# Performance work log

Hardware: AMD Instinct MI355X
Metric: run time of the kernel (lower is better)

Reference implementation:

```python
import jax, jax.numpy as jnp
import numpy as np

L, H, D, DK, FF = 3, 8, 128, 16, 512  # layers, heads, embed, key/val dim, ffn hidden
B, N, F_IN, OUT = 32, 512, 16, 3
SCALE = 1.0 / np.sqrt(DK)


def setup_inputs() -> dict:
    key = jax.random.key(0)
    ks = jax.random.split(key, 16)
    x = jax.random.normal(ks[0], (B, N, F_IN), dtype=jnp.float32)
    m = jax.random.randint(ks[1], (B, N, N), 0, 2).astype(jnp.int32)
    # guarantee each query attends to at least itself (avoid all -inf rows)
    m = jnp.maximum(m, jnp.eye(N, dtype=jnp.int32)[None])
    def u(k, shape, fan):
        s = 1.0 / np.sqrt(fan)
        return jax.random.uniform(k, shape, jnp.float32, -s, s)
    return {
        "x": x, "mask": m,
        "We": u(ks[2], (F_IN, D), D),
        "Wq": u(ks[3], (L, H, D, DK), DK),
        "Wk": u(ks[4], (L, H, D, DK), DK),
        "Wv": u(ks[5], (L, H, D, DK), DK),
        "Wout": u(ks[6], (L, H, DK, D), D),
        "Wff1": u(ks[7], (L, D, FF), D),
        "bff1": u(ks[8], (L, FF), D),
        "Wff2": u(ks[9], (L, FF, D), FF),
        "bff2": u(ks[10], (L, D), FF),
        "Wp": u(ks[11], (D, D), D),
        "Wr": u(ks[12], (2 * D, OUT), 2 * D),
        "br": u(ks[13], (OUT,), 2 * D),
    }


def reference(x, mask, We, Wq, Wk, Wv, Wout, Wff1, bff1, Wff2, bff2, Wp, Wr, br):
    mb = mask.astype(bool)[None]  # [1,B,N,N] broadcast over heads
    h = jax.nn.relu(x @ We)  # initial embedding [B,N,D]
    for l in range(L):
        # multi-head attention with additive skip
        Q = jnp.einsum('bnd,hdk->hbnk', h, Wq[l])
        K = jnp.einsum('bnd,hdk->hbnk', h, Wk[l])
        V = jnp.einsum('bnd,hdk->hbnk', h, Wv[l])
        compat = SCALE * jnp.einsum('hbqk,hbnk->hbqn', Q, K)  # [H,B,N,N]
        compat = jnp.where(mb, compat, -jnp.inf)
        attn = jax.nn.softmax(compat, axis=-1)
        # note: torch's attn.clone()[...] = 0 is a no-op, so no re-zeroing
        heads = jnp.einsum('hbqn,hbnk->hbqk', attn, V)
        h = h + jnp.einsum('hbqk,hkd->bqd', heads, Wout[l])
        # feed-forward with additive skip
        h = h + jax.nn.relu(h @ Wff1[l] + bff1[l]) @ Wff2[l] + bff2[l] * 0 + (jax.nn.relu(h @ Wff1[l] + bff1[l]) @ Wff2[l] + bff2[l] - (jax.nn.relu(h @ Wff1[l] + bff1[l]) @ Wff2[l]))  # placeholder removed below
    return h


# clean faithful version (used)
def reference(x, mask, We, Wq, Wk, Wv, Wout, Wff1, bff1, Wff2, bff2, Wp, Wr, br):
    mb = mask.astype(bool)[None]  # [1,B,N,N]
    h = jax.nn.relu(x @ We)  # [B,N,D]
    for l in range(L):
        Q = jnp.einsum('bnd,hdk->hbnk', h, Wq[l])
        K = jnp.einsum('bnd,hdk->hbnk', h, Wk[l])
        V = jnp.einsum('bnd,hdk->hbnk', h, Wv[l])
        compat = SCALE * jnp.einsum('hbqk,hbnk->hbqn', Q, K)
        compat = jnp.where(mb, compat, -jnp.inf)
        attn = jax.nn.softmax(compat, axis=-1)
        heads = jnp.einsum('hbqn,hbnk->hbqk', attn, V)
        h = h + jnp.einsum('hbqk,hkd->bqd', heads, Wout[l])
        h = h + (jax.nn.relu(h @ Wff1[l] + bff1[l]) @ Wff2[l] + bff2[l])
    # readout (actor head: output_dim=3)
    h_pooled = (h.mean(axis=1)) @ Wp  # [B,D]
    f_pooled = jnp.broadcast_to(h_pooled[:, None, :], h.shape)  # [B,N,D]
    features = jax.nn.relu(jnp.concatenate([f_pooled, h], axis=-1))  # [B,N,2D]
    return features @ Wr + br  # [B,N,3]
```

## Files before the change

### kernel.cpp

```cpp
#include <hip/hip_runtime.h>
#include <cstdint>
#include <cstddef>

#define L_LAYERS 3
#define H_HEADS 8
#define D_EMB 128
#define DKV 16
#define FF_DIM 512
#define B_BATCH 32
#define N_SEQ 512
#define F_INP 16
#define OUT_DIM 3
#define M_ROWS (B_BATCH * N_SEQ)
#define QSCALE 0.3606737602222409f

typedef unsigned short ushort_t;
typedef unsigned int uint_t;
typedef __attribute__((ext_vector_type(8))) short short8;
typedef __attribute__((ext_vector_type(4))) float f32x4;
typedef __attribute__((ext_vector_type(16))) float f32x16;

__device__ inline ushort_t f2bf(float x) {
    union { float f; uint_t u; } v; v.f = x;
    uint_t r = v.u + 0x7fffu + ((v.u >> 16) & 1u);
    return (ushort_t)(r >> 16);
}

__device__ inline uint_t pack2bf_tr(float a, float b) {
    union { float f; uint_t u; } ua, ub;
    ua.f = a; ub.f = b;
#if __has_builtin(__builtin_amdgcn_perm)
    return __builtin_amdgcn_perm(ub.u, ua.u, 0x07060302u);
#else
    return (ua.u >> 16) | (ub.u & 0xffff0000u);
#endif
}

__device__ inline float exp2fast(float x) {
#if __has_builtin(__builtin_amdgcn_exp2f)
    return __builtin_amdgcn_exp2f(x);
#else
    float r; __asm__("v_exp_f32 %0, %1" : "=v"(r) : "v"(x)); return r;
#endif
}

__device__ inline void gload16(const void* g, void* l) {
    __builtin_amdgcn_global_load_lds(
        (const __attribute__((address_space(1))) unsigned int*)g,
        (__attribute__((address_space(3))) unsigned int*)l, 16, 0, 0);
}

#define PM_BLK 2048
#define RQ_BLK 576
#define TW_BLK 192
#define T1_BLK 768
#define T2_BLK 768
#define PB_BLK 16
#define EM_BLK 1024
__global__ __launch_bounds__(256) void preproc_kernel(
        const int* __restrict__ mask, unsigned long long* __restrict__ pm,
        const float* __restrict__ Wq, const float* __restrict__ Wk,
        const float* __restrict__ Wv, ushort_t* __restrict__ wqkvT,
        const float* __restrict__ Wout, ushort_t* __restrict__ woutT,
        const float* __restrict__ Wff1, ushort_t* __restrict__ wff1T,
        const float* __restrict__ Wff2, ushort_t* __restrict__ wff2T,
        float* __restrict__ pbsum,
        const float* __restrict__ x, const float* __restrict__ We,
        float* __restrict__ hf, ushort_t* __restrict__ hb) {
    int bx = blockIdx.x;
    const int tid = threadIdx.x;
    if (bx < PM_BLK) {
#pragma unroll 4
        for (int it = 0; it < 16; ++it) {
            const int gid = (bx * 16 + it) * 256 + tid;
            const int v = mask[gid];
            const unsigned long long bal = __ballot(v != 0);
            if ((tid & 63) == 0) pm[gid >> 6] = bal;
        }
        return;
    }
    bx -= PM_BLK;
    if (bx < RQ_BLK) {
        int idx = bx * 256 + tid;
        int d = idx & 127;
        int n = (idx >> 7) % 384;
        int l = idx / (384 * 128);
        int proj = n >> 7, hh = (n & 127) >> 4, kk = n & 15;
        const float* src = proj == 0 ? Wq : proj == 1 ? Wk : Wv;
        wqkvT[idx] = f2bf(src[((size_t)(l * 8 + hh) * 128 + d) * 16 + kk]);
        return;
    }
    bx -= RQ_BLK;
    if (bx < TW_BLK + T1_BLK + T2_BLK) {
        const float* src; ushort_t* dst; int R, C;
        if (bx < TW_BLK) { src = Wout; dst = woutT; R = 128; C = 128; }
        else if (bx < TW_BLK + T1_BLK) { src = Wff1; dst = wff1T; R = 128; C = 512; bx -= TW_BLK; }
        else { src = Wff2; dst = wff2T; R = 512; C = 128; bx -= TW_BLK + T1_BLK; }
        int idx = bx * 256 + tid;
        int b = idx / (R * C);
        int rem = idx - b * (R * C);
        int c = rem / R, r = rem - c * R;
        dst[idx] = f2bf(src[((size_t)b * R + r) * C + c]);
        return;
    }
    bx -= TW_BLK + T1_BLK + T2_BLK;
    if (bx < PB_BLK) {
        pbsum[bx * 256 + tid] = 0.f;
        return;
    }
    bx -= PB_BLK;
    {
        const int d = tid & 127;
#pragma unroll 2
        for (int it = 0; it < 8; ++it) {
            const int m = (bx * 8 + it) * 2 + (tid >> 7);
            const float* xr = x + (size_t)m * 16;
            float acc = 0.f;
#pragma unroll
            for (int k = 0; k < 16; k++) acc += xr[k] * We[k * 128 + d];
            acc = fmaxf(acc, 0.f);
            hf[(size_t)m * 128 + d] = acc;
            hb[(size_t)m * 128 + d] = f2bf(acc);
        }
    }
}

__global__ __launch_bounds__(512, 2) void qkv_attn_kernel(
        const ushort_t* __restrict__ hb,
        const ushort_t* __restrict__ WqkvT,
        const uint_t* __restrict__ pm,
        ushort_t* __restrict__ Aout) {
    __shared__ __align__(16) ushort_t sm[43136];
    ushort_t* KF  = sm;
    ushort_t* Vt  = sm + 8192;
    ushort_t* Qs  = sm + 16512;
    ushort_t* Ws  = sm + 24704;
    ushort_t* PsA = sm + 24704;
    ushort_t* PsB = sm + 33920;

    const int tid = threadIdx.x;
    const int w = tid >> 6, L = tid & 63;
    const int lr = L & 15, lq = L >> 4;
    const int lane31 = L & 31, lhalf = L >> 5;
    const int bx = blockIdx.x;
    const int b = bx >> 3, h = bx & 7;

    for (int i = tid; i < 768; i += 512) {
        const int row = i >> 4, cg = i & 15;
        const int proj = row >> 4, kk = row & 15;
        gload16(WqkvT + (size_t)(proj * 128 + h * 16 + kk) * 128 + cg * 8, &Ws[i * 8]);
    }
    __syncthreads();

    const ushort_t* Ab = hb + (size_t)b * 512 * 128;
    for (int mc = 0; mc < 4; mc++) {
        f32x4 acc[3];
#pragma unroll
        for (int j = 0; j < 3; j++) acc[j] = (f32x4){0.f, 0.f, 0.f, 0.f};
#pragma unroll
        for (int k0 = 0; k0 < 128; k0 += 32) {
            short8 af = *(const short8*)(Ab + (size_t)(mc * 128 + w * 16 + lr) * 128 + k0 + lq * 8);
#pragma unroll
            for (int j = 0; j < 3; j++) {
                short8 bf = *(const short8*)&Ws[(j * 16 + lr) * 128 + k0 + lq * 8];
                acc[j] = __builtin_amdgcn_mfma_f32_16x16x32_bf16(af, bf, acc[j], 0, 0, 0);
            }
        }
        const int rbase = mc * 128 + w * 16 + lq * 4;
#pragma unroll
        for (int r = 0; r < 4; r++) {
            const int key = rbase + r;
            KF[(key >> 5) * 512 + ((lr >> 3) * 32 + (key & 31)) * 8 + (lr & 7)] = f2bf(acc[1][r]);
            Vt[lr * 520 + key] = f2bf(acc[2][r]);
            Qs[(key) * 16 + lr] = f2bf(acc[0][r] * QSCALE);
        }
    }
    __syncthreads();

    const f32x16 zero16 = (f32x16)(0.f);
    short8 vone;
#pragma unroll
    for (int i = 0; i < 8; i++) vone[i] = (short)0x3F80;

#define CS_STEP(T_IDX, PS) do {                                                     \
    short8 kf = *(const short8*)&KF[(T_IDX) * 512 + L * 8];                         \
    f32x16 s = __builtin_amdgcn_mfma_f32_32x32x16_bf16(kf, qf, zero16, 0, 0, 0);    \
    const uint_t word = mw[(T_IDX)];                                                \
    _Pragma("unroll")                                                               \
    for (int r = 0; r < 16; r++) {                                                  \
        const int keyl = (r & 3) + 8 * (r >> 2) + 4 * lhalf;                        \
        const float e = exp2fast(s[r]);                                             \
        s[r] = (word & (1u << keyl)) ? e : 0.f;                                     \
    }                                                                               \
    _Pragma("unroll")                                                               \
    for (int g = 0; g < 4; g++) {                                                   \
        const uint_t lo = pack2bf_tr(s[g * 4 + 0], s[g * 4 + 1]);                   \
        const uint_t hi = pack2bf_tr(s[g * 4 + 2], s[g * 4 + 3]);                   \
        *(uint2*)&(PS)[w * 1152 + lane31 * 36 + g * 8 + 4 * lhalf] = make_uint2(lo, hi); \
    }                                                                               \
} while (0)

#define PV_STEP(T_IDX, PS) do {                                                     \
    short8 vb = *(const short8*)&Vt[lr * 520 + (T_IDX) * 32 + lq * 8];              \
    short8 pa0 = *(const short8*)&(PS)[w * 1152 + lr * 36 + lq * 8];                \
    short8 pa1 = *(const short8*)&(PS)[w * 1152 + (16 + lr) * 36 + lq * 8];         \
    oacc0 = __builtin_amdgcn_mfma_f32_16x16x32_bf16(pa0, vb, oacc0, 0, 0, 0);       \
    oacc1 = __builtin_amdgcn_mfma_f32_16x16x32_bf16(pa1, vb, oacc1, 0, 0, 0);       \
    lacc0 = __builtin_amdgcn_mfma_f32_16x16x32_bf16(pa0, vone, lacc0, 0, 0, 0);     \
    lacc1 = __builtin_amdgcn_mfma_f32_16x16x32_bf16(pa1, vone, lacc1, 0, 0, 0);     \
} while (0)

#define PIPE_STEP(T_IDX, PSCUR, PSPREV) do {                                        \
    short8 kf = *(const short8*)&KF[(T_IDX) * 512 + L * 8];                         \
    f32x16 s = __builtin_amdgcn_mfma_f32_32x32x16_bf16(kf, qf, zero16, 0, 0, 0);    \
    PV_STEP((T_IDX) - 1, PSPREV);                                                   \
    const uint_t word = mw[(T_IDX)];                                                \
    _Pragma("unroll")                                                               \
    for (int r = 0; r < 16; r++) {                                                  \
        const int keyl = (r & 3) + 8 * (r >> 2) + 4 * lhalf;                        \
        const float e = exp2fast(s[r]);                                             \
        s[r] = (word & (1u << keyl)) ? e : 0.f;                                     \
    }                                                                               \
    _Pragma("unroll")                                                               \
    for (int g = 0; g < 4; g++) {                                                   \
        const uint_t lo = pack2bf_tr(s[g * 4 + 0], s[g * 4 + 1]);                   \
        const uint_t hi = pack2bf_tr(s[g * 4 + 2], s[g * 4 + 3]);                   \
        *(uint2*)&(PSCUR)[w * 1152 + lane31 * 36 + g * 8 + 4 * lhalf] = make_uint2(lo, hi); \
    }                                                                               \
} while (0)

    for (int qloop = 0; qloop < 2; ++qloop) {
        const int q0g = qloop * 256 + w * 32;
        const short8 qf = *(const short8*)&Qs[(q0g + lane31) * 16 + lhalf * 8];
        const uint_t* pmr = pm + (size_t)(b * 512 + q0g + lane31) * 16;
        const uint4 mwa = *(const uint4*)(pmr);
        const uint4 mwb = *(const uint4*)(pmr + 4);
        const uint4 mwc = *(const uint4*)(pmr + 8);
        const uint4 mwd = *(const uint4*)(pmr + 12);
        const uint_t mw[16] = {mwa.x, mwa.y, mwa.z, mwa.w, mwb.x, mwb.y, mwb.z, mwb.w,
                               mwc.x, mwc.y, mwc.z, mwc.w, mwd.x, mwd.y, mwd.z, mwd.w};

        f32x4 oacc0 = (f32x4){0.f, 0.f, 0.f, 0.f};
        f32x4 oacc1 = (f32x4){0.f, 0.f, 0.f, 0.f};
        f32x4 lacc0 = (f32x4){0.f, 0.f, 0.f, 0.f};
        f32x4 lacc1 = (f32x4){0.f, 0.f, 0.f, 0.f};

        CS_STEP(0, PsA);
#pragma unroll
        for (int tp = 0; tp < 7; tp++) {
            PIPE_STEP(2 * tp + 1, PsB, PsA);
            PIPE_STEP(2 * tp + 2, PsA, PsB);
        }
        PIPE_STEP(15, PsB, PsA);
        PV_STEP(15, PsB);

#pragma unroll
        for (int qa = 0; qa < 2; qa++) {
            const f32x4 oa = qa ? oacc1 : oacc0;
            const f32x4 la = qa ? lacc1 : lacc0;
#pragma unroll
            for (int rr = 0; rr < 4; rr++) {
                const int qloc = qa * 16 + lq * 4 + rr;
                Aout[(size_t)(b * 512 + q0g + qloc) * 128 + h * 16 + lr] = f2bf(oa[rr] / la[rr]);
            }
        }
    }
#undef CS_STEP
#undef PV_STEP
#undef PIPE_STEP
}

__global__ __launch_bounds__(256, 2) void tail_kernel(
        const ushort_t* __restrict__ A,
        const ushort_t* __restrict__ WoT,
        const ushort_t* __restrict__ W1T,
        const ushort_t* __restrict__ W2T,
        const float* __restrict__ b1,
        const float* __restrict__ b2,
        float* __restrict__ hf, ushort_t* __restrict__ hb,
        float* __restrict__ pbsum, int accum) {
    __shared__ __align__(16) ushort_t sm[39424];
    ushort_t* AsA = sm;
    ushort_t* AsB = sm + 1024;
    ushort_t* BsA = sm + 2048;
    ushort_t* BsB = sm + 10240;
    ushort_t* C1b = sm + 18432;
    ushort_t* T   = sm + 22784;

    const int tid = threadIdx.x;
    const int w = tid >> 6, l = tid & 63;
    const int lr = l & 15, lq = l >> 4;
    const int srow = (l >> 2);
    const int scol = (l & 3) * 8;
    const int m0 = blockIdx.x * 32;

    f32x4 c1a[2][2];
#pragma unroll
    for (int i = 0; i < 2; i++)
#pragma unroll
        for (int j = 0; j < 2; j++) c1a[i][j] = (f32x4){0.f, 0.f, 0.f, 0.f};
    if (w < 2)
        gload16(A + (size_t)(m0 + w * 16 + srow) * 128 + scol, &AsA[(w * 16 + srow) * 32 + scol]);
#pragma unroll
    for (int it = 0; it < 2; it++)
        gload16(WoT + (size_t)(it * 64 + w * 16 + srow) * 128 + scol, &BsA[(it * 64 + w * 16 + srow) * 32 + scol]);
#pragma unroll
    for (int k0 = 0; k0 < 128; k0 += 32) {
        ushort_t* Ac = (k0 & 32) ? AsB : AsA;
        ushort_t* Bc = (k0 & 32) ? BsB : BsA;
        ushort_t* An = (k0 & 32) ? AsA : AsB;
        ushort_t* Bn = (k0 & 32) ? BsA : BsB;
        __syncthreads();
        if (k0 + 32 < 128) {
            if (w < 2)
                gload16(A + (size_t)(m0 + w * 16 + srow) * 128 + k0 + 32 + scol,
                        &An[(w * 16 + srow) * 32 + scol]);
#pragma unroll
            for (int it = 0; it < 2; it++)
                gload16(WoT + (size_t)(it * 64 + w * 16 + srow) * 128 + k0 + 32 + scol,
                        &Bn[(it * 64 + w * 16 + srow) * 32 + scol]);
        }
        short8 af[2], bfr[2];
#pragma unroll
        for (int i = 0; i < 2; i++) af[i] = *(const short8*)&Ac[(i * 16 + lr) * 32 + lq * 8];
#pragma unroll
        for (int j = 0; j < 2; j++) bfr[j] = *(const short8*)&Bc[(w * 32 + j * 16 + lr) * 32 + lq * 8];
#pragma unroll
        for (int i = 0; i < 2; i++)
#pragma unroll
            for (int j = 0; j < 2; j++)
                c1a[i][j] = __builtin_amdgcn_mfma_f32_16x16x32_bf16(af[i], bfr[j], c1a[i][j], 0, 0, 0);
    }
    float c1[2][2][4];
#pragma unroll
    for (int i = 0; i < 2; i++)
#pragma unroll
        for (int r = 0; r < 4; r++) {
            const int row = i * 16 + lq * 4 + r;
#pragma unroll
            for (int j = 0; j < 2; j++) {
                const int n = w * 32 + j * 16 + lr;
                const float v = c1a[i][j][r] + hf[(size_t)(m0 + row) * 128 + n];
                c1[i][j][r] = v;
                C1b[row * 136 + n] = f2bf(v);
            }
        }

#pragma unroll
    for (int it = 0; it < 4; it++)
        gload16(W1T + (size_t)(it * 64 + w * 16 + srow) * 128 + scol, &BsA[(it * 64 + w * 16 + srow) * 32 + scol]);
#pragma unroll
    for (int nc = 0; nc < 2; nc++) {
        f32x4 ta[2][4];
#pragma unroll
        for (int i = 0; i < 2; i++)
#pragma unroll
            for (int j = 0; j < 4; j++) ta[i][j] = (f32x4){0.f, 0.f, 0.f, 0.f};
#pragma unroll
        for (int k0i = 0; k0i < 4; k0i++) {
            const int c = nc * 4 + k0i;
            ushort_t* Bc = (c & 1) ? BsB : BsA;
            ushort_t* Bn = (c & 1) ? BsA : BsB;
            __syncthreads();
            if (c + 1 < 8) {
                const int nc2 = (c + 1) >> 2, k02 = ((c + 1) & 3) * 32;
#pragma unroll
                for (int it = 0; it < 4; it++)
                    gload16(W1T + (size_t)(nc2 * 256 + it * 64 + w * 16 + srow) * 128 + k02 + scol,
                            &Bn[(it * 64 + w * 16 + srow) * 32 + scol]);
            }
            short8 af[2], bfr[4];
#pragma unroll
            for (int i = 0; i < 2; i++)
                af[i] = *(const short8*)&C1b[(i * 16 + lr) * 136 + k0i * 32 + lq * 8];
#pragma unroll
            for (int j = 0; j < 4; j++)
                bfr[j] = *(const short8*)&Bc[(w * 64 + j * 16 + lr) * 32 + lq * 8];
#pragma unroll
            for (int i = 0; i < 2; i++)
#pragma unroll
                for (int j = 0; j < 4; j++)
                    ta[i][j] = __builtin_amdgcn_mfma_f32_16x16x32_bf16(af[i], bfr[j], ta[i][j], 0, 0, 0);
        }
#pragma unroll
        for (int j = 0; j < 4; j++) {
            const int n = nc * 256 + w * 64 + j * 16 + lr;
            const float bv = b1[n];
#pragma unroll
            for (int i = 0; i < 2; i++)
#pragma unroll
                for (int r = 0; r < 4; r++) {
                    const int row = i * 16 + lq * 4 + r;
                    T[row * 520 + n] = f2bf(fmaxf(ta[i][j][r] + bv, 0.f));
                }
        }
    }

#pragma unroll
    for (int it = 0; it < 2; it++)
        gload16(W2T + (size_t)(it * 64 + w * 16 + srow) * 512 + scol, &BsA[(it * 64 + w * 16 + srow) * 32 + scol]);
    f32x4 oa[2][2];
#pragma unroll
    for (int i = 0; i < 2; i++)
#pragma unroll
        for (int j = 0; j < 2; j++) oa[i][j] = (f32x4){0.f, 0.f, 0.f, 0.f};
#pragma unroll
    for (int k0 = 0; k0 < 512; k0 += 32) {
        ushort_t* Bc = ((k0 >> 5) & 1) ? BsB : BsA;
        ushort_t* Bn = ((k0 >> 5) & 1) ? BsA : BsB;
        __syncthreads();
        if (k0 + 32 < 512) {
#pragma unroll
            for (int it = 0; it < 2; it++)
                gload16(W2T + (size_t)(it * 64 + w * 16 + srow) * 512 + k0 + 32 + scol,
                        &Bn[(it * 64 + w * 16 + srow) * 32 + scol]);
        }
        short8 af[2], bfr[2];
#pragma unroll
        for (int i = 0; i < 2; i++)
            af[i] = *(const short8*)&T[(i * 16 + lr) * 520 + k0 + lq * 8];
#pragma unroll
        for (int j = 0; j < 2; j++)
            bfr[j] = *(const short8*)&Bc[(w * 32 + j * 16 + lr) * 32 + lq * 8];
#pragma unroll
        for (int i = 0; i < 2; i++)
#pragma unroll
            for (int j = 0; j < 2; j++)
                oa[i][j] = __builtin_amdgcn_mfma_f32_16x16x32_bf16(af[i], bfr[j], oa[i][j], 0, 0, 0);
    }
#pragma unroll
    for (int j = 0; j < 2; j++) {
        const int n = w * 32 + j * 16 + lr;
        const float bv = b2[n];
        float psum = 0.f;
#pragma unroll
        for (int i = 0; i < 2; i++)
#pragma unroll
            for (int r = 0; r < 4; r++) {
                const int row = i * 16 + lq * 4 + r;
                const float v = oa[i][j][r] + bv + c1[i][j][r];
                psum += v;
                hf[(size_t)(m0 + row) * 128 + n] = v;
                hb[(size_t)(m0 + row) * 128 + n] = f2bf(v);
            }
        if (accum) {
            psum += __shfl_xor(psum, 16);
            psum += __shfl_xor(psum, 32);
            if (lq == 0) atomicAdd(&pbsum[(m0 >> 9) * 128 + n], psum);
        }
    }
}

__global__ __launch_bounds__(256) void readout_kernel(const float* __restrict__ h,
                                                      const float* __restrict__ pbsum,
                                                      const float* __restrict__ Wp,
                                                      const float* __restrict__ Wr,
                                                      const float* __restrict__ br,
                                                      float* __restrict__ out) {
    const int u = blockIdx.x;
    const int b = u >> 4;
    const int m0 = u * 32;
    const int t = threadIdx.x;
    __shared__ float pooled[128];
    __shared__ float rp[128];
    __shared__ float pb3[3];
    if (t < 128) pooled[t] = pbsum[b * 128 + t] * (1.0f / 512.0f);
    __syncthreads();
    if (t < 128) {
        float a = 0.f;
        for (int dd = 0; dd < 128; dd++) a += pooled[dd] * Wp[dd * 128 + t];
        rp[t] = fmaxf(a, 0.f);
    }
    __syncthreads();
    if (t < OUT_DIM) {
        float a = br[t];
        for (int j = 0; j < 128; j++) a += rp[j] * Wr[j * 3 + t];
        pb3[t] = a;
    }
    __syncthreads();
    const int j = t & 7;
    const int row = m0 + (t >> 3);
    const float* hr = h + (size_t)row * 128 + j * 16;
    float a0 = 0.f, a1 = 0.f, a2o = 0.f;
#pragma unroll
    for (int dd = 0; dd < 16; dd++) {
        const float v = fmaxf(hr[dd], 0.f);
        const float* wr = Wr + (size_t)(128 + j * 16 + dd) * 3;
        a0 += v * wr[0]; a1 += v * wr[1]; a2o += v * wr[2];
    }
#pragma unroll
    for (int off = 4; off; off >>= 1) {
        a0 += __shfl_down(a0, off, 8);
        a1 += __shfl_down(a1, off, 8);
        a2o += __shfl_down(a2o, off, 8);
    }
    if (j == 0) {
        out[(size_t)row * 3 + 0] = a0 + pb3[0];
        out[(size_t)row * 3 + 1] = a1 + pb3[1];
        out[(size_t)row * 3 + 2] = a2o + pb3[2];
    }
}

extern "C" void kernel_launch(void* const* d_in, const int* in_sizes, int n_in,
                              void* d_out, int out_size, void* d_ws, size_t ws_size,
                              hipStream_t stream) {
    const float* x    = (const float*)d_in[0];
    const int*   mask = (const int*)d_in[1];
    const float* We   = (const float*)d_in[2];
    const float* Wq   = (const float*)d_in[3];
    const float* Wk   = (const float*)d_in[4];
    const float* Wv   = (const float*)d_in[5];
    const float* Wout = (const float*)d_in[6];
    const float* Wff1 = (const float*)d_in[7];
    const float* bff1 = (const float*)d_in[8];
    const float* Wff2 = (const float*)d_in[9];
    const float* bff2 = (const float*)d_in[10];
    const float* Wp   = (const float*)d_in[11];
    const float* Wr   = (const float*)d_in[12];
    const float* br   = (const float*)d_in[13];
    float* out = (float*)d_out;

    char* ws = (char*)d_ws;
    unsigned long long* pm64 = (unsigned long long*)(ws + 0);
    const uint_t* pm32       = (const uint_t*)(ws + 0);
    ushort_t* wqkvT = (ushort_t*)(ws + 1048576);
    ushort_t* woutT = (ushort_t*)(ws + 1343488);
    ushort_t* wff1T = (ushort_t*)(ws + 1441792);
    ushort_t* wff2T = (ushort_t*)(ws + 1835008);
    float*    pbsum = (float*)(ws + 2228224);
    float*    hbuf  = (float*)(ws + 4194304);
    ushort_t* hb16  = (ushort_t*)(ws + 12582912);
    ushort_t* a16   = (ushort_t*)(ws + 41943040);

    preproc_kernel<<<PM_BLK + RQ_BLK + TW_BLK + T1_BLK + T2_BLK + PB_BLK + EM_BLK, 256, 0, stream>>>(
        mask, pm64, Wq, Wk, Wv, wqkvT, Wout, woutT, Wff1, wff1T, Wff2, wff2T,
        pbsum, x, We, hbuf, hb16);

    for (int l = 0; l < L_LAYERS; l++) {
        qkv_attn_kernel<<<256, 512, 0, stream>>>(
            hb16, wqkvT + (size_t)l * 384 * 128, pm32, a16);
        tail_kernel<<<M_ROWS / 32, 256, 0, stream>>>(
            a16, woutT + (size_t)l * 128 * 128, wff1T + (size_t)l * 512 * 128,
            wff2T + (size_t)l * 128 * 512, bff1 + l * 512, bff2 + l * 128,
            hbuf, hb16, pbsum, (l == L_LAYERS - 1) ? 1 : 0);
    }

    readout_kernel<<<512, 256, 0, stream>>>(hbuf, pbsum, Wp, Wr, br, out);
}
```

Before: 265.6 us.

## Deepen attention software pipeline to three stages with triple-buffered P tiles

Restructures the per-tile attention loop in qkv_attn_kernel so that QK^T for tile T, PV for tile T-2, and exp/mask/write for tile T-1 are interleaved. Score registers are double-buffered and the shared-memory P buffer is tripled. The aim is to give MFMA results more time to land before the exp stage, and LDS writes more time before the PV reads, so fewer pipeline stalls occur. In exchange it uses more registers (two f32x16 score tiles live) and about 18KB more LDS, which could reduce occupancy under launch_bounds(512,2).

```diff
diff --git a/kernel.cpp b/kernel.cpp
--- a/kernel.cpp
+++ b/kernel.cpp
@@ -130,13 +130,14 @@
         const ushort_t* __restrict__ WqkvT,
         const uint_t* __restrict__ pm,
         ushort_t* __restrict__ Aout) {
-    __shared__ __align__(16) ushort_t sm[43136];
+    __shared__ __align__(16) ushort_t sm[52352];
     ushort_t* KF  = sm;
     ushort_t* Vt  = sm + 8192;
     ushort_t* Qs  = sm + 16512;
     ushort_t* Ws  = sm + 24704;
-    ushort_t* PsA = sm + 24704;
-    ushort_t* PsB = sm + 33920;
+    ushort_t* Ps0 = sm + 24704;
+    ushort_t* Ps1 = sm + 33920;
+    ushort_t* Ps2 = sm + 43136;
 
     const int tid = threadIdx.x;
     const int w = tid >> 6, L = tid & 63;
@@ -182,9 +183,15 @@
 #pragma unroll
     for (int i = 0; i < 8; i++) vone[i] = (short)0x3F80;
 
-#define CS_STEP(T_IDX, PS) do {                                                     \
+#define PSB(i) ((i) == 0 ? Ps0 : (i) == 1 ? Ps1 : Ps2)
+
+#define QK_STEP(T_IDX) do {                                                         \
     short8 kf = *(const short8*)&KF[(T_IDX) * 512 + L * 8];                         \
-    f32x16 s = __builtin_amdgcn_mfma_f32_32x32x16_bf16(kf, qf, zero16, 0, 0, 0);    \
+    sreg[(T_IDX) & 1] = __builtin_amdgcn_mfma_f32_32x32x16_bf16(kf, qf, zero16, 0, 0, 0); \
+} while (0)
+
+#define EXPW_STEP(T_IDX) do {                                                       \
+    f32x16 s = sreg[(T_IDX) & 1];                                                   \
     const uint_t word = mw[(T_IDX)];                                                \
     _Pragma("unroll")                                                               \
     for (int r = 0; r < 16; r++) {                                                  \
@@ -192,41 +199,24 @@
         const float e = exp2fast(s[r]);                                             \
         s[r] = (word & (1u << keyl)) ? e : 0.f;                                     \
     }                                                                               \
+    ushort_t* PS = PSB((T_IDX) % 3);                                                \
     _Pragma("unroll")                                                               \
     for (int g = 0; g < 4; g++) {                                                   \
         const uint_t lo = pack2bf_tr(s[g * 4 + 0], s[g * 4 + 1]);                   \
         const uint_t hi = pack2bf_tr(s[g * 4 + 2], s[g * 4 + 3]);                   \
-        *(uint2*)&(PS)[w * 1152 + lane31 * 36 + g * 8 + 4 * lhalf] = make_uint2(lo, hi); \
+        *(uint2*)&PS[w * 1152 + lane31 * 36 + g * 8 + 4 * lhalf] = make_uint2(lo, hi); \
     }                                                                               \
 } while (0)
 
-#define PV_STEP(T_IDX, PS) do {                                                     \
+#define PV_STEP(T_IDX) do {                                                         \
+    ushort_t* PS = PSB((T_IDX) % 3);                                                \
     short8 vb = *(const short8*)&Vt[lr * 520 + (T_IDX) * 32 + lq * 8];              \
-    short8 pa0 = *(const short8*)&(PS)[w * 1152 + lr * 36 + lq * 8];                \
-    short8 pa1 = *(const short8*)&(PS)[w * 1152 + (16 + lr) * 36 + lq * 8];         \
+    short8 pa0 = *(const short8*)&PS[w * 1152 + lr * 36 + lq * 8];                  \
+    short8 pa1 = *(const short8*)&PS[w * 1152 + (16 + lr) * 36 + lq * 8];           \
     oacc0 = __builtin_amdgcn_mfma_f32_16x16x32_bf16(pa0, vb, oacc0, 0, 0, 0);       \
     oacc1 = __builtin_amdgcn_mfma_f32_16x16x32_bf16(pa1, vb, oacc1, 0, 0, 0);       \
     lacc0 = __builtin_amdgcn_mfma_f32_16x16x32_bf16(pa0, vone, lacc0, 0, 0, 0);     \
     lacc1 = __builtin_amdgcn_mfma_f32_16x16x32_bf16(pa1, vone, lacc1, 0, 0, 0);     \
-} while (0)
-
-#define PIPE_STEP(T_IDX, PSCUR, PSPREV) do {                                        \
-    short8 kf = *(const short8*)&KF[(T_IDX) * 512 + L * 8];                         \
-    f32x16 s = __builtin_amdgcn_mfma_f32_32x32x16_bf16(kf, qf, zero16, 0, 0, 0);    \
-    PV_STEP((T_IDX) - 1, PSPREV);                                                   \
-    const uint_t word = mw[(T_IDX)];                                                \
-    _Pragma("unroll")                                                               \
-    for (int r = 0; r < 16; r++) {                                                  \
-        const int keyl = (r & 3) + 8 * (r >> 2) + 4 * lhalf;                        \
-        const float e = exp2fast(s[r]);                                             \
-        s[r] = (word & (1u << keyl)) ? e : 0.f;                                     \
-    }                                                                               \
-    _Pragma("unroll")                                                               \
-    for (int g = 0; g < 4; g++) {                                                   \
-        const uint_t lo = pack2bf_tr(s[g * 4 + 0], s[g * 4 + 1]);                   \
-        const uint_t hi = pack2bf_tr(s[g * 4 + 2], s[g * 4 + 3]);                   \
-        *(uint2*)&(PSCUR)[w * 1152 + lane31 * 36 + g * 8 + 4 * lhalf] = make_uint2(lo, hi); \
-    }                                                                               \
 } while (0)
 
     for (int qloop = 0; qloop < 2; ++qloop) {
@@ -244,15 +234,18 @@
         f32x4 oacc1 = (f32x4){0.f, 0.f, 0.f, 0.f};
         f32x4 lacc0 = (f32x4){0.f, 0.f, 0.f, 0.f};
         f32x4 lacc1 = (f32x4){0.f, 0.f, 0.f, 0.f};
-
-        CS_STEP(0, PsA);
-#pragma unroll
-        for (int tp = 0; tp < 7; tp++) {
-            PIPE_STEP(2 * tp + 1, PsB, PsA);
-            PIPE_STEP(2 * tp + 2, PsA, PsB);
-        }
-        PIPE_STEP(15, PsB, PsA);
-        PV_STEP(15, PsB);
+        f32x16 sreg[2];
+
+        QK_STEP(0);
+        QK_STEP(1); EXPW_STEP(0);
+#pragma unroll
+        for (int T = 2; T <= 15; ++T) {
+            QK_STEP(T);
+            PV_STEP(T - 2);
+            EXPW_STEP(T - 1);
+        }
+        PV_STEP(14); EXPW_STEP(15);
+        PV_STEP(15);
 
 #pragma unroll
         for (int qa = 0; qa < 2; qa++) {
@@ -265,9 +258,10 @@
             }
         }
     }
-#undef CS_STEP
+#undef QK_STEP
+#undef EXPW_STEP
 #undef PV_STEP
-#undef PIPE_STEP
+#undef PSB
 }
 
 __global__ __launch_bounds__(256, 2) void tail_kernel(
```

Result: slower. 279.2 us (+5.1%).
